# Kernel tuning notes

Hardware: AMD Instinct MI355X
Metric: run time of the kernel (lower is better)

## Reference

```python
import jax, jax.numpy as jnp
import numpy as np

N = 50000      # nodes
E = 800000     # edges
IN_DIM = 256
D = 32         # out_dim per head
H = 8          # num_heads
NEG_SLOPE = 0.01  # torch F.leaky_relu default


def setup_inputs() -> dict:
    key = jax.random.key(0)
    k1, k2, k3, k4, k5 = jax.random.split(key, 5)
    h = jax.random.normal(k1, (N, IN_DIM), dtype=jnp.float32)
    W = jax.random.normal(k2, (H, IN_DIM, D), dtype=jnp.float32) * 0.05
    attn_w = jax.random.normal(k3, (H, 2 * D), dtype=jnp.float32) * 0.05
    src = jax.random.randint(k4, (E,), 0, N, dtype=jnp.int64)
    dst = jax.random.randint(k5, (E,), 0, N, dtype=jnp.int64)
    return {"h": h, "W": W, "attn_w": attn_w, "src": src, "dst": dst}


def reference(h, W, attn_w, src, dst):
    # per-head linear projection: z[n,h,d]
    z = jnp.einsum('ni,hid->nhd', h, W)
    # attn_fc(concat(z_src, z_dst)) = z_src @ a_l + z_dst @ a_r
    a_l, a_r = attn_w[:, :D], attn_w[:, D:]
    el = jnp.einsum('nhd,hd->nh', z, a_l)  # [N,H]
    er = jnp.einsum('nhd,hd->nh', z, a_r)  # [N,H]
    e = jax.nn.leaky_relu(el[src] + er[dst], NEG_SLOPE)  # [E,H]
    # segment softmax over incoming edges of each destination node
    m = jax.ops.segment_max(e, dst, num_segments=N)      # [N,H]
    m = jnp.where(jnp.isfinite(m), m, 0.0)               # nodes w/ no in-edges
    num = jnp.exp(e - m[dst])                            # [E,H]
    den = jax.ops.segment_sum(num, dst, num_segments=N)  # [N,H]
    den_e = den[dst]
    alpha = num / jnp.where(den_e > 0, den_e, 1.0)       # [E,H]
    # weighted scatter-sum of source features
    msg = alpha[:, :, None] * z[src]                     # [E,H,D]
    hout = jax.ops.segment_sum(msg, dst, num_segments=N) # [N,H,D]
    # merge='cat': concat head outputs along feature dim
    return hout.reshape(N, H * D)
```

## Files before the change

kernel.cpp:

```cpp
#include <hip/hip_runtime.h>
#include <math.h>

#define NN 50000
#define EE 800000
#define INDIM 256
#define DD 32
#define HH 8
#define CC 256
#define NEG 0.01f
#define NSCAN 49

typedef __attribute__((ext_vector_type(8))) short bf16x8;
typedef __attribute__((ext_vector_type(4))) float f32x4;

__device__ __forceinline__ unsigned short f32_to_bf16_rne(float f) {
  unsigned u = __float_as_uint(f);
  u += 0x7fffu + ((u >> 16) & 1u);
  return (unsigned short)(u >> 16);
}
__device__ __forceinline__ float bf16_to_f32(unsigned short b) {
  return __uint_as_float((unsigned)b << 16);
}

__global__ __launch_bounds__(256) void k_prep(const unsigned* __restrict__ sraw,
                                              const unsigned* __restrict__ draw,
                                              int* __restrict__ s32, int* __restrict__ d32,
                                              unsigned short* __restrict__ slot,
                                              int* __restrict__ counts,
                                              const float* __restrict__ W,
                                              unsigned short* __restrict__ WbT) {
  __shared__ int sflag;
  if (threadIdx.x == 0) sflag = 0;
  __syncthreads();
  const int gt = blockIdx.x * 256 + threadIdx.x;
  unsigned v = 0;
#pragma unroll
  for (int i = 0; i < 4; ++i) {
    int e = (gt * 4 + i) % (EE / 2);
    v |= sraw[2 * e + 1] | draw[2 * e + 1];
  }
  if (v) atomicOr(&sflag, 1);
  __syncthreads();
  const int is32 = sflag;

  const int stride = gridDim.x * blockDim.x;
  for (int e = gt; e < EE; e += stride) {
    int sv, dv;
    if (is32) {
      sv = ((const int*)sraw)[e];
      dv = ((const int*)draw)[e];
    } else {
      sv = (int)((const long long*)sraw)[e];
      dv = (int)((const long long*)draw)[e];
    }
    s32[e] = sv;
    d32[e] = dv;
    slot[e] = (unsigned short)atomicAdd(&counts[dv], 1);
  }

  if (gt < INDIM * CC) {
    int n = gt >> 8, k = gt & 255;
    int hh = n >> 5, d = n & 31;
    WbT[gt] = f32_to_bf16_rne(W[(size_t)hh * 8192 + k * 32 + d]);
  }
}

__global__ __launch_bounds__(512) void k_gemm(const float* __restrict__ h,
                                              const unsigned short* __restrict__ WbT,
                                              const float* __restrict__ attn_w,
                                              unsigned short* __restrict__ z,
                                              float* __restrict__ el,
                                              float* __restrict__ er) {
  __shared__ short sA[64 * 256];
  const int t = threadIdx.x;
  const int l = t & 63;
  const int w = t >> 6;
  const int row0 = blockIdx.x * 64;

#pragma unroll
  for (int i = 0; i < 4; ++i) {
    int q = i * 512 + t;
    int row = q >> 5, c = q & 31;
    int grow = row0 + row; if (grow >= NN) grow = NN - 1;
    const float* src = &h[(size_t)grow * 256 + c * 8];
    float4 f0 = *reinterpret_cast<const float4*>(src);
    float4 f1 = *reinterpret_cast<const float4*>(src + 4);
    bf16x8 vv;
    vv[0] = (short)f32_to_bf16_rne(f0.x); vv[1] = (short)f32_to_bf16_rne(f0.y);
    vv[2] = (short)f32_to_bf16_rne(f0.z); vv[3] = (short)f32_to_bf16_rne(f0.w);
    vv[4] = (short)f32_to_bf16_rne(f1.x); vv[5] = (short)f32_to_bf16_rne(f1.y);
    vv[6] = (short)f32_to_bf16_rne(f1.z); vv[7] = (short)f32_to_bf16_rne(f1.w);
    int sc = c ^ (row & 7);
    *reinterpret_cast<bf16x8*>(&sA[row * 256 + sc * 8]) = vv;
  }

  bf16x8 bf[2][8];
  {
    const int n = w * 32 + (l & 15);
    const int kb = (l >> 4) * 8;
#pragma unroll
    for (int c = 0; c < 2; ++c)
#pragma unroll
      for (int kk = 0; kk < 8; ++kk)
        bf[c][kk] = *reinterpret_cast<const bf16x8*>(
            &WbT[(size_t)(n + c * 16) * 256 + kk * 32 + kb]);
  }

  f32x4 acc[4][2];
#pragma unroll
  for (int m = 0; m < 4; ++m)
#pragma unroll
    for (int c = 0; c < 2; ++c) acc[m][c] = (f32x4){0.f, 0.f, 0.f, 0.f};

  __syncthreads();

#pragma unroll
  for (int kk = 0; kk < 8; ++kk) {
    bf16x8 af[4];
#pragma unroll
    for (int m = 0; m < 4; ++m) {
      int row = m * 16 + (l & 15);
      int chunk = kk * 4 + (l >> 4);
      int sc = chunk ^ (row & 7);
      af[m] = *reinterpret_cast<const bf16x8*>(&sA[row * 256 + sc * 8]);
    }
#pragma unroll
    for (int m = 0; m < 4; ++m)
#pragma unroll
      for (int c = 0; c < 2; ++c)
        acc[m][c] = __builtin_amdgcn_mfma_f32_16x16x32_bf16(bf[c][kk], af[m], acc[m][c], 0, 0, 0);
  }

#pragma unroll
  for (int m = 0; m < 4; ++m) {
    int node = row0 + m * 16 + (l & 15);
    if (node < NN) {
#pragma unroll
      for (int c = 0; c < 2; ++c) {
        ushort4 pk;
        pk.x = f32_to_bf16_rne(acc[m][c][0]);
        pk.y = f32_to_bf16_rne(acc[m][c][1]);
        pk.z = f32_to_bf16_rne(acc[m][c][2]);
        pk.w = f32_to_bf16_rne(acc[m][c][3]);
        *reinterpret_cast<ushort4*>(
            &z[(size_t)node * CC + w * 32 + c * 16 + ((l >> 4) << 2)]) = pk;
      }
    }
  }

  float alc[2][4], arc[2][4];
#pragma unroll
  for (int c = 0; c < 2; ++c)
#pragma unroll
    for (int r = 0; r < 4; ++r) {
      int d = c * 16 + ((l >> 4) << 2) + r;
      alc[c][r] = attn_w[w * 64 + d];
      arc[c][r] = attn_w[w * 64 + 32 + d];
    }
#pragma unroll
  for (int m = 0; m < 4; ++m) {
    float pl = 0.f, pr = 0.f;
#pragma unroll
    for (int c = 0; c < 2; ++c)
#pragma unroll
      for (int r = 0; r < 4; ++r) {
        pl += acc[m][c][r] * alc[c][r];
        pr += acc[m][c][r] * arc[c][r];
      }
    pl += __shfl_xor(pl, 16); pl += __shfl_xor(pl, 32);
    pr += __shfl_xor(pr, 16); pr += __shfl_xor(pr, 32);
    if ((l >> 4) == 0) {
      int node = row0 + m * 16 + l;
      if (node < NN) {
        el[(size_t)node * HH + w] = pl;
        er[(size_t)node * HH + w] = pr;
      }
    }
  }
}

__global__ __launch_bounds__(1024) void k_scan(const int* __restrict__ counts,
                                               int* __restrict__ row_start,
                                               int* __restrict__ partial) {
  __shared__ int s[1024];
  const int tid = threadIdx.x;
  const int i = blockIdx.x * 1024 + tid;
  int v = (i < NN) ? counts[i] : 0;
  s[tid] = v;
  __syncthreads();
  for (int off = 1; off < 1024; off <<= 1) {
    int tv = (tid >= off) ? s[tid - off] : 0;
    __syncthreads();
    s[tid] += tv;
    __syncthreads();
  }
  if (i < NN) row_start[i] = s[tid] - v;
  if (tid == 1023) partial[blockIdx.x] = s[1023];
}

__device__ __forceinline__ void block_base_scan(const int* __restrict__ partial,
                                                int* __restrict__ sbase) {
  if (threadIdx.x < 64) {
    int l = threadIdx.x;
    int x = (l < NSCAN) ? partial[l] : 0;
    int orig = x;
#pragma unroll
    for (int off = 1; off < 64; off <<= 1) {
      int y = __shfl_up(x, off);
      if (l >= off) x += y;
    }
    sbase[l] = x - orig;
  }
  __syncthreads();
}

__global__ __launch_bounds__(256) void k_scatter(const int* __restrict__ s32,
                                                 const int* __restrict__ d32,
                                                 const unsigned short* __restrict__ slot,
                                                 const int* __restrict__ row_start,
                                                 const int* __restrict__ partial,
                                                 int* __restrict__ csr_src) {
  __shared__ int sbase[64];
  block_base_scan(partial, sbase);
  int stride = gridDim.x * blockDim.x;
  for (int e = blockIdx.x * blockDim.x + threadIdx.x; e < EE; e += stride) {
    int dn = d32[e];
    int pos = row_start[dn] + sbase[dn >> 10] + (int)slot[e];
    csr_src[pos] = s32[e];
  }
}

#define AGG_WAVES 8192
__global__ __launch_bounds__(256) void k_agg(const unsigned short* __restrict__ z,
                                             const float* __restrict__ el,
                                             const float* __restrict__ er,
                                             const int* __restrict__ row_start,
                                             const int* __restrict__ partial,
                                             const int* __restrict__ csr_src,
                                             float* __restrict__ out) {
  __shared__ int sbase[64];
  block_base_scan(partial, sbase);

  const int gw = blockIdx.x * 4 + (threadIdx.x >> 6);
  const int l = threadIdx.x & 63;
  const int head = l >> 3;

  for (int n = gw; n < NN; n += AGG_WAVES) {
    const int beg = row_start[n] + sbase[n >> 10];
    const int end = (n == NN - 1) ? EE : (row_start[n + 1] + sbase[(n + 1) >> 10]);
    const float ern = er[(size_t)n * HH + head];

    float den = 0.f;
    float a0 = 0.f, a1 = 0.f, a2 = 0.f, a3 = 0.f;
#pragma unroll 4
    for (int p = beg; p < end; ++p) {
      int s = csr_src[p];
      float v = el[(size_t)s * HH + head] + ern;
      v = (v > 0.f) ? v : v * NEG;
      float wgt = __expf(v);
      ushort4 zv = *reinterpret_cast<const ushort4*>(&z[(size_t)s * CC + 4 * l]);
      den += wgt;
      a0 += wgt * bf16_to_f32(zv.x);
      a1 += wgt * bf16_to_f32(zv.y);
      a2 += wgt * bf16_to_f32(zv.z);
      a3 += wgt * bf16_to_f32(zv.w);
    }
    const float rd = (end > beg) ? (1.f / den) : 0.f;
    float4 o;
    o.x = a0 * rd; o.y = a1 * rd; o.z = a2 * rd; o.w = a3 * rd;
    *reinterpret_cast<float4*>(&out[(size_t)n * CC + 4 * l]) = o;
  }
}

extern "C" void kernel_launch(void* const* d_in, const int* in_sizes, int n_in,
                              void* d_out, int out_size, void* d_ws, size_t ws_size,
                              hipStream_t stream) {
  const float* h      = (const float*)d_in[0];
  const float* W      = (const float*)d_in[1];
  const float* attn_w = (const float*)d_in[2];
  const void*  src_raw = d_in[3];
  const void*  dst_raw = d_in[4];
  float* out = (float*)d_out;

  char* ws = (char*)d_ws;
  size_t off = 0;
  unsigned short* z   = (unsigned short*)(ws + off); off += (size_t)NN * CC * 2;
  unsigned short* WbT = (unsigned short*)(ws + off); off += (size_t)INDIM * CC * 2;
  float* el = (float*)(ws + off); off += (size_t)NN * HH * 4;
  float* er = (float*)(ws + off); off += (size_t)NN * HH * 4;
  int* counts    = (int*)(ws + off); off += (size_t)NN * 4;
  int* row_start = (int*)(ws + off); off += (size_t)NN * 4;
  int* partial   = (int*)(ws + off); off += 256;
  int* s32  = (int*)(ws + off); off += (size_t)EE * 4;
  int* d32  = (int*)(ws + off); off += (size_t)EE * 4;
  unsigned short* slot = (unsigned short*)(ws + off); off += (size_t)EE * 2;
  int* csr_src = (int*)(ws + off); off += (size_t)EE * 4;

  hipMemsetAsync(counts, 0, (size_t)NN * 4, stream);

  k_prep<<<1024, 256, 0, stream>>>((const unsigned*)src_raw, (const unsigned*)dst_raw,
                                   s32, d32, slot, counts, W, WbT);

  k_gemm<<<(NN + 63) / 64, 512, 0, stream>>>(h, WbT, attn_w, z, el, er);

  k_scan<<<NSCAN, 1024, 0, stream>>>(counts, row_start, partial);

  k_scatter<<<2048, 256, 0, stream>>>(s32, d32, slot, row_start, partial, csr_src);

  k_agg<<<AGG_WAVES / 4, 256, 0, stream>>>(z, el, er, row_start, partial, csr_src, out);
}
```

Baseline: 167.9 us.

## Replicate degree counters eight ways and narrow edge indices to 16-bit

```diff
diff --git a/kernel.cpp b/kernel.cpp
--- a/kernel.cpp
+++ b/kernel.cpp
@@ -8,7 +8,10 @@
 #define HH 8
 #define CC 256
 #define NEG 0.01f
+#define NREP 8
 #define NSCAN 49
+#define PREP_GRID 1024
+#define PREP_STRIDE (PREP_GRID * 256)
 
 typedef __attribute__((ext_vector_type(8))) short bf16x8;
 typedef __attribute__((ext_vector_type(4))) float f32x4;
@@ -24,9 +27,10 @@
 
 __global__ __launch_bounds__(256) void k_prep(const unsigned* __restrict__ sraw,
                                               const unsigned* __restrict__ draw,
-                                              int* __restrict__ s32, int* __restrict__ d32,
-                                              unsigned short* __restrict__ slot,
-                                              int* __restrict__ counts,
+                                              int* __restrict__ counts8,
+                                              unsigned short* __restrict__ s16,
+                                              unsigned short* __restrict__ d16,
+                                              unsigned short* __restrict__ slot16,
                                               const float* __restrict__ W,
                                               unsigned short* __restrict__ WbT) {
   __shared__ int sflag;
@@ -43,8 +47,10 @@
   __syncthreads();
   const int is32 = sflag;
 
-  const int stride = gridDim.x * blockDim.x;
-  for (int e = gt; e < EE; e += stride) {
+  const int rep = blockIdx.x & (NREP - 1);
+  int* __restrict__ mycounts = counts8 + rep * NN;
+
+  for (int e = gt; e < EE; e += PREP_STRIDE) {
     int sv, dv;
     if (is32) {
       sv = ((const int*)sraw)[e];
@@ -53,9 +59,9 @@
       sv = (int)((const long long*)sraw)[e];
       dv = (int)((const long long*)draw)[e];
     }
-    s32[e] = sv;
-    d32[e] = dv;
-    slot[e] = (unsigned short)atomicAdd(&counts[dv], 1);
+    s16[e] = (unsigned short)sv;
+    d16[e] = (unsigned short)dv;
+    slot16[e] = (unsigned short)atomicAdd(&mycounts[dv], 1);
   }
 
   if (gt < INDIM * CC) {
@@ -179,14 +185,29 @@
   }
 }
 
-__global__ __launch_bounds__(1024) void k_scan(const int* __restrict__ counts,
+__global__ __launch_bounds__(1024) void k_scan(const int* __restrict__ counts8,
                                                int* __restrict__ row_start,
-                                               int* __restrict__ partial) {
+                                               int* __restrict__ partial,
+                                               unsigned char* __restrict__ offs8) {
   __shared__ int s[1024];
   const int tid = threadIdx.x;
   const int i = blockIdx.x * 1024 + tid;
-  int v = (i < NN) ? counts[i] : 0;
-  s[tid] = v;
+  int deg = 0;
+  if (i < NN) {
+    unsigned pack0 = 0, pack1 = 0;
+    int run = 0;
+#pragma unroll
+    for (int r = 0; r < NREP; ++r) {
+      int c = counts8[r * NN + i];
+      if (r < 4) pack0 |= (unsigned)run << (8 * r);
+      else       pack1 |= (unsigned)run << (8 * (r - 4));
+      run += c;
+    }
+    deg = run;
+    uint2 pk; pk.x = pack0; pk.y = pack1;
+    *reinterpret_cast<uint2*>(&offs8[(size_t)i * 8]) = pk;
+  }
+  s[tid] = deg;
   __syncthreads();
   for (int off = 1; off < 1024; off <<= 1) {
     int tv = (tid >= off) ? s[tid - off] : 0;
@@ -194,7 +215,7 @@
     s[tid] += tv;
     __syncthreads();
   }
-  if (i < NN) row_start[i] = s[tid] - v;
+  if (i < NN) row_start[i] = s[tid] - deg;
   if (tid == 1023) partial[blockIdx.x] = s[1023];
 }
 
@@ -214,19 +235,21 @@
   __syncthreads();
 }
 
-__global__ __launch_bounds__(256) void k_scatter(const int* __restrict__ s32,
-                                                 const int* __restrict__ d32,
-                                                 const unsigned short* __restrict__ slot,
+__global__ __launch_bounds__(256) void k_scatter(const unsigned short* __restrict__ s16,
+                                                 const unsigned short* __restrict__ d16,
+                                                 const unsigned short* __restrict__ slot16,
+                                                 const unsigned char* __restrict__ offs8,
                                                  const int* __restrict__ row_start,
                                                  const int* __restrict__ partial,
-                                                 int* __restrict__ csr_src) {
+                                                 unsigned short* __restrict__ csr16) {
   __shared__ int sbase[64];
   block_base_scan(partial, sbase);
   int stride = gridDim.x * blockDim.x;
   for (int e = blockIdx.x * blockDim.x + threadIdx.x; e < EE; e += stride) {
-    int dn = d32[e];
-    int pos = row_start[dn] + sbase[dn >> 10] + (int)slot[e];
-    csr_src[pos] = s32[e];
+    int dn = (int)d16[e];
+    int rep = ((e & (PREP_STRIDE - 1)) >> 8) & (NREP - 1);
+    int pos = row_start[dn] + sbase[dn >> 10] + (int)offs8[dn * 8 + rep] + (int)slot16[e];
+    csr16[pos] = s16[e];
   }
 }
 
@@ -236,7 +259,7 @@
                                              const float* __restrict__ er,
                                              const int* __restrict__ row_start,
                                              const int* __restrict__ partial,
-                                             const int* __restrict__ csr_src,
+                                             const unsigned short* __restrict__ csr16,
                                              float* __restrict__ out) {
   __shared__ int sbase[64];
   block_base_scan(partial, sbase);
@@ -254,7 +277,7 @@
     float a0 = 0.f, a1 = 0.f, a2 = 0.f, a3 = 0.f;
 #pragma unroll 4
     for (int p = beg; p < end; ++p) {
-      int s = csr_src[p];
+      int s = (int)csr16[p];
       float v = el[(size_t)s * HH + head] + ern;
       v = (v > 0.f) ? v : v * NEG;
       float wgt = __expf(v);
@@ -288,24 +311,25 @@
   unsigned short* WbT = (unsigned short*)(ws + off); off += (size_t)INDIM * CC * 2;
   float* el = (float*)(ws + off); off += (size_t)NN * HH * 4;
   float* er = (float*)(ws + off); off += (size_t)NN * HH * 4;
-  int* counts    = (int*)(ws + off); off += (size_t)NN * 4;
+  int* counts8 = (int*)(ws + off); off += (size_t)NREP * NN * 4;
   int* row_start = (int*)(ws + off); off += (size_t)NN * 4;
   int* partial   = (int*)(ws + off); off += 256;
-  int* s32  = (int*)(ws + off); off += (size_t)EE * 4;
-  int* d32  = (int*)(ws + off); off += (size_t)EE * 4;
-  unsigned short* slot = (unsigned short*)(ws + off); off += (size_t)EE * 2;
-  int* csr_src = (int*)(ws + off); off += (size_t)EE * 4;
-
-  hipMemsetAsync(counts, 0, (size_t)NN * 4, stream);
-
-  k_prep<<<1024, 256, 0, stream>>>((const unsigned*)src_raw, (const unsigned*)dst_raw,
-                                   s32, d32, slot, counts, W, WbT);
+  unsigned char* offs8 = (unsigned char*)(ws + off); off += (size_t)NN * 8;
+  unsigned short* s16    = (unsigned short*)(ws + off); off += (size_t)EE * 2;
+  unsigned short* d16    = (unsigned short*)(ws + off); off += (size_t)EE * 2;
+  unsigned short* slot16 = (unsigned short*)(ws + off); off += (size_t)EE * 2;
+  unsigned short* csr16  = (unsigned short*)(ws + off); off += (size_t)EE * 2;
+
+  hipMemsetAsync(counts8, 0, (size_t)NREP * NN * 4, stream);
+
+  k_prep<<<PREP_GRID, 256, 0, stream>>>((const unsigned*)src_raw, (const unsigned*)dst_raw,
+                                        counts8, s16, d16, slot16, W, WbT);
 
   k_gemm<<<(NN + 63) / 64, 512, 0, stream>>>(h, WbT, attn_w, z, el, er);
 
-  k_scan<<<NSCAN, 1024, 0, stream>>>(counts, row_start, partial);
-
-  k_scatter<<<2048, 256, 0, stream>>>(s32, d32, slot, row_start, partial, csr_src);
-
-  k_agg<<<AGG_WAVES / 4, 256, 0, stream>>>(z, el, er, row_start, partial, csr_src, out);
-}
+  k_scan<<<NSCAN, 1024, 0, stream>>>(counts8, row_start, partial, offs8);
+
+  k_scatter<<<2048, 256, 0, stream>>>(s16, d16, slot16, offs8, row_start, partial, csr16);
+
+  k_agg<<<AGG_WAVES / 4, 256, 0, stream>>>(z, el, er, row_start, partial, csr16, out);
+}
```

Measured after the change: 166.1 us. No clear change (-1.1%).
